# Optimization experiments

Measured on AMD Instinct MI355X. Metric: run time of the kernel, lower is better.

## Reference

```python
import jax, jax.numpy as jnp
import numpy as np

U = 256      # lstm_unit / embedding_fc_unit
V = 100000   # word vocab
WD = 300     # word embedding dim
PD = 64      # pos embedding dim
AD = 64      # action embedding dim
P = 50       # pos vocab
NA = 164     # 4 + 4*dep_num actions
B, T, K, L, S, A, DQ = 64, 128, 4, 128, 64, 64, 32
FORGET_BIAS = 1.0


def lstm_step(x, c, h, W, b):
    z = jnp.concatenate([x, h], -1) @ W + b
    i, j, f, o = jnp.split(z, 4, -1)
    nc = c * jax.nn.sigmoid(f + FORGET_BIAS) + jax.nn.sigmoid(i) * jnp.tanh(j)
    nh = jnp.tanh(nc) * jax.nn.sigmoid(o)
    return nc, nh


def run_lstm(xs, length, W, b):
    # xs: [B, L, D]; TF dynamic_rnn semantics: state frozen and output zeroed past length.
    Bn, Ln, _ = xs.shape
    u = W.shape[1] // 4
    def step(carry, tx):
        c, h = carry
        t, x = tx
        nc, nh = lstm_step(x, c, h, W, b)
        m = (t < length)[:, None]
        return (jnp.where(m, nc, c), jnp.where(m, nh, h)), jnp.where(m, nh, 0.0)
    init = (jnp.zeros((Bn, u), xs.dtype), jnp.zeros((Bn, u), xs.dtype))
    (cf, hf), outs = jax.lax.scan(step, init, (jnp.arange(Ln), jnp.swapaxes(xs, 0, 1)))
    return jnp.swapaxes(outs, 0, 1), (cf, hf)


def reverse_seq(xs, length):
    # tf.reverse_sequence: reverse first `length` steps, leave the rest in place.
    Ln = xs.shape[1]
    t = jnp.arange(Ln)[None, :]
    rev = jnp.where(t < length[:, None], length[:, None] - 1 - t, t)
    return jnp.take_along_axis(xs, rev[:, :, None], axis=1)


def forward(tree_word_id, tree_pos_id, token_word_id, token_pos_id, history_action_id,
            buff_top_id, deque_word_id, deque_pos_id, deque_length, children_order,
            stack_order, stack_length, token_length, history_action_length,
            word_emb, pos_emb, act_emb, wd_W, wd_b, tree_W, tree_b,
            stack0_W, stack0_b, stack1_W, stack1_b,
            fw0_W, fw0_b, bw0_W, bw0_b, fw1_W, fw1_b, bw1_W, bw1_b,
            act0_W, act0_b, act1_W, act1_b, dq0_W, dq0_b, dq1_W, dq1_b,
            fin_W, fin_b):
    Bn = tree_word_id.shape[0]

    def embed(wid, pid):
        e = jnp.concatenate([word_emb[wid], pos_emb[pid]], -1)
        return jax.nn.relu(e @ wd_W + wd_b)

    tree_e = embed(tree_word_id, tree_pos_id)       # [B, T, U]
    token_e = embed(token_word_id, token_pos_id)    # [B, L, U]
    deque_e = embed(deque_word_id, deque_pos_id)    # [B, DQ, U]
    hist_e = act_emb[history_action_id]             # [B, A, AD]

    # ---- tree LSTM over children structure ----
    Tn = tree_e.shape[1]
    Kn = children_order.shape[2]
    batch_col = jnp.arange(Bn)[:, None]
    H0 = jnp.zeros((Tn + 1, Bn, U), tree_e.dtype)
    C0 = jnp.zeros((Tn + 1, Bn, U), tree_e.dtype)

    def body(carry, i):
        H, C = carry
        idx = children_order[:, i]            # [B, K] indices into slots 0..i
        h = H[idx, batch_col]                 # [B, K, U]
        c = C[idx, batch_col]
        x = tree_e[:, i]                      # [B, U]
        hj = h.sum(1)
        ijo = jnp.concatenate([x, hj], -1) @ tree_W[:, :3 * U] + tree_b[:3 * U]
        xk = jnp.broadcast_to(x[:, None, :], (Bn, Kn, x.shape[-1]))
        f = jnp.concatenate([xk, h], -1) @ tree_W[:, 3 * U:] + tree_b[3 * U:]   # [B, K, U]
        ig, jg, og = jnp.split(ijo, 3, -1)
        nc = (c * jax.nn.sigmoid(f + FORGET_BIAS)).sum(1) + jax.nn.sigmoid(ig) * jnp.tanh(jg)
        nh = jnp.tanh(nc) * jax.nn.sigmoid(og)
        return (H.at[i + 1].set(nh), C.at[i + 1].set(nc)), None

    (H, _), _ = jax.lax.scan(body, (H0, C0), jnp.arange(Tn))
    stack_embedded = H[stack_order, batch_col]      # [B, S, U]

    # ---- stack LSTM (2-layer) ----
    o0, _ = run_lstm(stack_embedded, stack_length, stack0_W, stack0_b)
    _, (_, stack_h) = run_lstm(o0, stack_length, stack1_W, stack1_b)

    # ---- buff bi-LSTM (2 stacked bidirectional layers) ----
    fw0_o, _ = run_lstm(token_e, token_length, fw0_W, fw0_b)
    bw0_o, _ = run_lstm(reverse_seq(token_e, token_length), token_length, bw0_W, bw0_b)
    bw0_o = reverse_seq(bw0_o, token_length)
    x1 = jnp.concatenate([fw0_o, bw0_o], -1)
    fw1_o, (_, fw1_h) = run_lstm(x1, token_length, fw1_W, fw1_b)
    bw1_o, _ = run_lstm(reverse_seq(x1, token_length), token_length, bw1_W, bw1_b)
    bw1_o = reverse_seq(bw1_o, token_length)
    bidx = jnp.arange(Bn)
    fw_top = fw1_o[bidx, buff_top_id]
    bw_top = bw1_o[bidx, buff_top_id]
    bw_bottom = bw1_o[bidx, token_length - 1]
    buff_out = jnp.concatenate([fw1_h - fw_top, bw_top - bw_bottom], -1)

    # ---- action LSTM (2-layer) ----
    a0, _ = run_lstm(hist_e, history_action_length, act0_W, act0_b)
    _, (_, act_h) = run_lstm(a0, history_action_length, act1_W, act1_b)

    # ---- deque LSTM (2-layer) ----
    d0, _ = run_lstm(deque_e, deque_length, dq0_W, dq0_b)
    _, (_, dq_h) = run_lstm(d0, deque_length, dq1_W, dq1_b)

    feat = jnp.concatenate([stack_h, buff_out, act_h, dq_h], -1)   # [B, 5U]
    return jax.nn.relu(feat @ fin_W + fin_b)


def setup_inputs():
    key = jax.random.key(0)
    ks = jax.random.split(key, 48)
    r = lambda i, shape: jax.random.normal(ks[i], shape, jnp.float32) * 0.05
    ri = lambda i, shape, hi: jax.random.randint(ks[i], shape, 0, hi)
    inp = {}
    inp['tree_word_id'] = ri(0, (B, T), V)
    inp['tree_pos_id'] = ri(1, (B, T), P)
    inp['token_word_id'] = ri(2, (B, L), V)
    inp['token_pos_id'] = ri(3, (B, L), P)
    inp['history_action_id'] = ri(4, (B, A), NA)
    inp['buff_top_id'] = ri(5, (B,), L // 2)
    inp['deque_word_id'] = ri(6, (B, DQ), V)
    inp['deque_pos_id'] = ri(7, (B, DQ), P)
    inp['deque_length'] = jax.random.randint(ks[8], (B,), 1, DQ + 1)
    co = ri(9, (B, T, K), T)
    # a node may only reference already-computed children slots (<= step index)
    inp['children_order'] = jnp.minimum(co, jnp.arange(T)[None, :, None])
    inp['stack_order'] = ri(10, (B, S), T + 1)
    inp['stack_length'] = jax.random.randint(ks[11], (B,), 1, S + 1)
    inp['token_length'] = jax.random.randint(ks[12], (B,), L // 2, L + 1)
    inp['history_action_length'] = jax.random.randint(ks[13], (B,), 1, A + 1)
    inp['word_emb'] = r(14, (V, WD))
    inp['pos_emb'] = r(15, (P, PD))
    inp['act_emb'] = r(16, (NA, AD))
    inp['wd_W'] = r(17, (WD + PD, U)); inp['wd_b'] = jnp.zeros((U,))
    inp['tree_W'] = r(18, (2 * U, 4 * U)); inp['tree_b'] = jnp.zeros((4 * U,))
    inp['stack0_W'] = r(19, (2 * U, 4 * U)); inp['stack0_b'] = jnp.zeros((4 * U,))
    inp['stack1_W'] = r(20, (2 * U, 4 * U)); inp['stack1_b'] = jnp.zeros((4 * U,))
    inp['fw0_W'] = r(21, (2 * U, 4 * U)); inp['fw0_b'] = jnp.zeros((4 * U,))
    inp['bw0_W'] = r(22, (2 * U, 4 * U)); inp['bw0_b'] = jnp.zeros((4 * U,))
    inp['fw1_W'] = r(23, (3 * U, 4 * U)); inp['fw1_b'] = jnp.zeros((4 * U,))
    inp['bw1_W'] = r(24, (3 * U, 4 * U)); inp['bw1_b'] = jnp.zeros((4 * U,))
    inp['act0_W'] = r(25, (AD + U, 4 * U)); inp['act0_b'] = jnp.zeros((4 * U,))
    inp['act1_W'] = r(26, (2 * U, 4 * U)); inp['act1_b'] = jnp.zeros((4 * U,))
    inp['dq0_W'] = r(27, (2 * U, 4 * U)); inp['dq0_b'] = jnp.zeros((4 * U,))
    inp['dq1_W'] = r(28, (2 * U, 4 * U)); inp['dq1_b'] = jnp.zeros((4 * U,))
    inp['fin_W'] = r(29, (5 * U, NA)); inp['fin_b'] = jnp.zeros((NA,))
    return inp


def reference(tree_word_id, tree_pos_id, token_word_id, token_pos_id, history_action_id,
              buff_top_id, deque_word_id, deque_pos_id, deque_length, children_order,
              stack_order, stack_length, token_length, history_action_length,
              word_emb, pos_emb, act_emb, wd_W, wd_b, tree_W, tree_b,
              stack0_W, stack0_b, stack1_W, stack1_b,
              fw0_W, fw0_b, bw0_W, bw0_b, fw1_W, fw1_b, bw1_W, bw1_b,
              act0_W, act0_b, act1_W, act1_b, dq0_W, dq0_b, dq1_W, dq1_b,
              fin_W, fin_b):
    return forward(tree_word_id, tree_pos_id, token_word_id, token_pos_id, history_action_id,
                   buff_top_id, deque_word_id, deque_pos_id, deque_length, children_order,
                   stack_order, stack_length, token_length, history_action_length,
                   word_emb, pos_emb, act_emb, wd_W, wd_b, tree_W, tree_b,
                   stack0_W, stack0_b, stack1_W, stack1_b,
                   fw0_W, fw0_b, bw0_W, bw0_b, fw1_W, fw1_b, bw1_W, bw1_b,
                   act0_W, act0_b, act1_W, act1_b, dq0_W, dq0_b, dq1_W, dq1_b,
                   fin_W, fin_b)
```

## Files before the change

### kernel.cpp

```cpp
#include <hip/hip_runtime.h>
#include <hip/hip_bf16.h>
#include <hip/hip_fp16.h>
#include <cstdint>

#define BB   64
#define TT   128
#define KK   4
#define LL   128
#define SS   64
#define AA   64
#define DQN  32
#define UU   256
#define NAOUT 164
#define WDIM 300
#define PDIM 64
#define ADIM 64

#define OFF_TREE 0
#define OFF_S0   512
#define OFF_S1   1024
#define OFF_FW0  1536
#define OFF_BW0  2048
#define OFF_FW1  2560
#define OFF_BW1  3328
// ... 177 lines not shown
    __shared__ __align__(16) float s_e[384];
    if (p.flag[0] == 1) embed_impl<true>(p, s_e);
    else                embed_impl<false>(p, s_e);
}

template<int R>
__device__ __forceinline__ float lstm_step_f4(const float4* __restrict__ Wp,
                                              const float4 bz,
                                              const float* __restrict__ s_xh,
                                              float& c) {
    float zi = bz.x, zj = bz.y, zf = bz.z, zo = bz.w;
    for (int r0 = 0; r0 < R; r0 += 16) {
        float4 w[16];
        #pragma unroll
        for (int k = 0; k < 16; ++k) w[k] = Wp[(size_t)(r0 + k) * 256];
        __builtin_amdgcn_sched_barrier(0);
        #pragma unroll
        for (int q = 0; q < 4; ++q) {
            const float4 x4 = *reinterpret_cast<const float4*>(s_xh + r0 + 4 * q);
            const float xv[4] = {x4.x, x4.y, x4.z, x4.w};
            #pragma unroll
            for (int j = 0; j < 4; ++j) {
                const float4 wv = w[4 * q + j];
                zi = fmaf(xv[j], wv.x, zi);
                zj = fmaf(xv[j], wv.y, zj);
                zf = fmaf(xv[j], wv.z, zf);
                zo = fmaf(xv[j], wv.w, zo);
            }
        }
    }
    const float nc = c * sigm(zf) + sigm(zi) * tanhf(zj);
    c = nc;
    return tanhf(nc) * sigm(zo);
}

template<bool F32>
__device__ __forceinline__ float4 load_bias4(const void* b, int u) {
    return make_float4(ld1<F32>(b, u), ld1<F32>(b, 256 + u),
                       ld1<F32>(b, 512 + u) + 1.0f, ld1<F32>(b, 768 + u));
}

__device__ __forceinline__ float4 zx_load(const uint2* __restrict__ zx, size_t n, int u) {
    const uint2 v = zx[n * 256 + u];
    const float2 ij = unp2h(v.x);
    const float2 fo = unp2h(v.y);
    return make_float4(ij.x, ij.y, fo.x, fo.y);
}

template<bool F32>
__device__ void run_tree_f4(int b, const P& p, float* smem) {
    const int u = threadIdx.x;
    float* s_x  = smem;
    float* s_hj = smem + 256;
    float* s_hk = smem + 512;
    float* H = p.H;
    float* C = p.C;
    H[(size_t)b * UU + u] = 0.f;
    C[(size_t)b * UU + u] = 0.f;

    const float4* __restrict__ Wt = p.pkf + u;
    const float4* __restrict__ Wh = Wt + (size_t)256 * 256;
    const float bi = ld1<F32>(p.tree_b, u);
    const float bj = ld1<F32>(p.tree_b, 256 + u);
    const float bo = ld1<F32>(p.tree_b, 512 + u);
    const float bf = ld1<F32>(p.tree_b, 768 + u) + 1.0f;

// ... 48 lines not shown
                const float4 hj4 = *reinterpret_cast<const float4*>(s_hj + r);
                const float4 a0  = *reinterpret_cast<const float4*>(s_hk + r);
                const float4 a1  = *reinterpret_cast<const float4*>(s_hk + 256 + r);
                const float4 a2  = *reinterpret_cast<const float4*>(s_hk + 512 + r);
                const float4 a3  = *reinterpret_cast<const float4*>(s_hk + 768 + r);
                const float hjv[4] = {hj4.x, hj4.y, hj4.z, hj4.w};
                const float k0[4]  = {a0.x, a0.y, a0.z, a0.w};
                const float k1[4]  = {a1.x, a1.y, a1.z, a1.w};
                const float k2[4]  = {a2.x, a2.y, a2.z, a2.w};
                const float k3[4]  = {a3.x, a3.y, a3.z, a3.w};
                #pragma unroll
                for (int j = 0; j < 4; ++j) {
                    const float4 wv = w[4 * q + j];
                    zi = fmaf(hjv[j], wv.x, zi);
                    zj = fmaf(hjv[j], wv.y, zj);
                    zo = fmaf(hjv[j], wv.z, zo);
                    f0 = fmaf(k0[j], wv.w, f0);
                    f1 = fmaf(k1[j], wv.w, f1);
                    f2 = fmaf(k2[j], wv.w, f2);
                    f3 = fmaf(k3[j], wv.w, f3);
                }
            }
        }
        const float fsum = c0 * sigm(fx + f0) + c1 * sigm(fx + f1)
                         + c2 * sigm(fx + f2) + c3 * sigm(fx + f3);
        const float nc = fsum + sigm(zi) * tanhf(zj);
        const float nh = tanhf(nc) * sigm(zo);
        __syncthreads();
        H[((size_t)(i + 1) * BB + b) * UU + u] = nh;
        C[((size_t)(i + 1) * BB + b) * UU + u] = nc;
    }
}

template<bool F32>
__device__ void run_tree_hc(int b, const P& p, float* smem) {
    const int u = threadIdx.x;
    float* s_hj = smem;
    float* s_hk = smem + 256;
    float* H = p.H;
    float* C = p.C;
    H[(size_t)b * UU + u] = 0.f;
    C[(size_t)b * UU + u] = 0.f;
    const float4* __restrict__ Wh = p.pkf + (size_t)256 * 256 + u;

    for (int i = 0; i < TT; ++i) {
        const int* co = p.children_order + ((size_t)b * TT + i) * KK;
        const int i0 = co[0], i1 = co[1], i2 = co[2], i3 = co[3];
        const float h0 = H[((size_t)i0 * BB + b) * UU + u];
        const float h1 = H[((size_t)i1 * BB + b) * UU + u];
        const float h2 = H[((size_t)i2 * BB + b) * UU + u];
        const float h3 = H[((size_t)i3 * BB + b) * UU + u];
        const float c0 = C[((size_t)i0 * BB + b) * UU + u];
        const float c1 = C[((size_t)i1 * BB + b) * UU + u];
        const float c2 = C[((size_t)i2 * BB + b) * UU + u];
        const float c3 = C[((size_t)i3 * BB + b) * UU + u];
        s_hk[u]       = h0;
        s_hk[256 + u] = h1;
        s_hk[512 + u] = h2;
        s_hk[768 + u] = h3;
        s_hj[u]       = h0 + h1 + h2 + h3;
        __syncthreads();

        const float4 z0 = p.zxT[((size_t)b * TT + i) * 256 + u];
        float zi = z0.x, zj = z0.y, zo = z0.z, fx = z0.w;
        float f0 = 0.f, f1 = 0.f, f2 = 0.f, f3 = 0.f;
        for (int r0 = 0; r0 < 256; r0 += 16) {
            float4 w[16];
            #pragma unroll
            for (int k = 0; k < 16; ++k) w[k] = Wh[(size_t)(r0 + k) * 256];
            __builtin_amdgcn_sched_barrier(0);
            #pragma unroll
            for (int q = 0; q < 4; ++q) {
                const int r = r0 + 4 * q;
                const float4 hj4 = *reinterpret_cast<const float4*>(s_hj + r);
                const float4 a0  = *reinterpret_cast<const float4*>(s_hk + r);
                const float4 a1  = *reinterpret_cast<const float4*>(s_hk + 256 + r);
                const float4 a2  = *reinterpret_cast<const float4*>(s_hk + 512 + r);
                const float4 a3  = *reinterpret_cast<const float4*>(s_hk + 768 + r);
                const float hjv[4] = {hj4.x, hj4.y, hj4.z, hj4.w};
                const float k0[4]  = {a0.x, a0.y, a0.z, a0.w};
                const float k1[4]  = {a1.x, a1.y, a1.z, a1.w};
                const float k2[4]  = {a2.x, a2.y, a2.z, a2.w};
                const float k3[4]  = {a3.x, a3.y, a3.z, a3.w};
                #pragma unroll
                for (int j = 0; j < 4; ++j) {
                    const float4 wv = w[4 * q + j];
                    zi = fmaf(hjv[j], wv.x, zi);
                    zj = fmaf(hjv[j], wv.y, zj);
                    zo = fmaf(hjv[j], wv.z, zo);
                    f0 = fmaf(k0[j], wv.w, f0);
                    f1 = fmaf(k1[j], wv.w, f1);
                    f2 = fmaf(k2[j], wv.w, f2);
                    f3 = fmaf(k3[j], wv.w, f3);
                }
            }
        }
        const float fsum = c0 * sigm(fx + f0) + c1 * sigm(fx + f1)
                         + c2 * sigm(fx + f2) + c3 * sigm(fx + f3);
        const float nc = fsum + sigm(zi) * tanhf(zj);
        const float nh = tanhf(nc) * sigm(zo);
        __syncthreads();
        H[((size_t)(i + 1) * BB + b) * UU + u] = nh;
        C[((size_t)(i + 1) * BB + b) * UU + u] = nc;
    }
}

template<bool F32>
__device__ void run_token_l0_f4(int b, const P& p, float* smem, bool is_bw) {
    const int u = threadIdx.x;
    float* s_xh = smem;
    const int len = p.token_length[b];
    const float4* __restrict__ Wp = p.pkf + (size_t)(is_bw ? OFF_BW0 : OFF_FW0) * 256 + u;
    const float4 bz = load_bias4<F32>(is_bw ? p.bw0_b : p.fw0_b, u);

    float c0 = 0.f;
    s_xh[256 + u] = 0.f;
    for (int t = 0; t < len; ++t) {
        const int row = is_bw ? (len - 1 - t) : t;
        s_xh[u] = bf2f(p.token_e[((size_t)b * LL + row) * UU + u]);
        __syncthreads();
        const float nh = lstm_step_f4<512>(Wp, bz, s_xh, c0);
        p.x1[((size_t)b * LL + row) * 512 + (is_bw ? 256 : 0) + u] = f2bf(nh);
        __syncthreads();
        s_xh[256 + u] = nh;
    }
}

template<bool F32>
__device__ void run_act_dq_f4(int b, const P& p, float* smem) {
    const int u = threadIdx.x;
    float* s_xh0 = smem;
    float* s_xh1 = smem + 512;

    {
        const int len = p.history_action_length[b];
        const float4* __restrict__ W0 = p.pkf + (size_t)OFF_ACT0 * 256 + u;
// ... 429 lines not shown
    float c = 0.f, hlast = 0.f;
    s_h[u] = 0.f;
    __syncthreads();
    for (int t = 0; t < len; ++t) {
        const float4 bz = zx_load(p.zxC, (size_t)b * AA + t, u);
        const float nh = lstm_step_f4<256>(Wh, bz, s_h, c);
        __syncthreads();
        s_h[u] = nh;
        __syncthreads();
        hlast = nh;
    }
    p.act_h[b * UU + u] = hlast;
}

template<bool F32>
__device__ void chain_dq1(int b, const P& p, float* s_h) {
    const int u = threadIdx.x;
    const int len = p.deque_length[b];
    const float4* __restrict__ Wh = p.pkf + (size_t)PKH_DQ1 * 256 + u;
    float c = 0.f, hlast = 0.f;
    s_h[u] = 0.f;
    __syncthreads();
    for (int t = 0; t < len; ++t) {
        const float4 bz = zx_load(p.zxD, (size_t)b * DQN + t, u);
        const float nh = lstm_step_f4<256>(Wh, bz, s_h, c);
        __syncthreads();
        s_h[u] = nh;
        __syncthreads();
        hlast = nh;
    }
    p.dq_h[b * UU + u] = hlast;
}

template<bool F32>
__device__ void p1b_impl(const P& p, float* smem) {
    const int chain = blockIdx.x >> 6;
    const int b     = blockIdx.x & 63;
    if (chain == 0)      run_tree_f4<F32>(b, p, smem);
    else if (chain == 1) chain_token_l0<F32>(b, p, smem, false);
    else if (chain == 2) chain_token_l0<F32>(b, p, smem, true);
    else if (chain == 3) chain_act0<F32>(b, p, smem);
    else                 chain_dq0<F32>(b, p, smem);
}

__global__ __launch_bounds__(256) void p1b_kernel(P p) {
    __shared__ __align__(16) float smem[1536];
    if (p.flag[0] == 1) p1b_impl<true>(p, smem);
    else                p1b_impl<false>(p, smem);
}

template<bool F32>
__device__ void p2b_impl(const P& p, float* smem) {
    const int chain = blockIdx.x >> 6;
    const int b     = blockIdx.x & 63;
    if (chain == 0)      chain_fw1<F32>(b, p, smem);
    else if (chain == 1) chain_bw1<F32>(b, p, smem);
    else if (chain == 2) chain_stack0<F32>(b, p, smem);
    else if (chain == 3) chain_act1<F32>(b, p, smem);
    else                 chain_dq1<F32>(b, p, smem);
}

__global__ __launch_bounds__(256) void p2b_kernel(P p) {
    __shared__ __align__(16) float smem[256];
    if (p.flag[0] == 1) p2b_impl<true>(p, smem);
    else                p2b_impl<false>(p, smem);
}

template<bool F32>
__device__ void p1c_impl(const P& p, float* smem) {
    const int s = blockIdx.x & 7;
    const int j = blockIdx.x >> 3;
    if (s == 0 || s == 5) {
        if (j >= 32) return;
        run_tree_hc<F32>((s == 5 ? 32 : 0) + j, p, smem);
    } else if (s == 1 || s == 6) {
        if (j >= 32) return;
        chain_token_l0<F32>((s == 6 ? 32 : 0) + j, p, smem, false);
    } else if (s == 2 || s == 7) {
        if (j >= 32) return;
        chain_token_l0<F32>((s == 7 ? 32 : 0) + j, p, smem, true);
    } else if (s == 3) {
        chain_act0<F32>(j, p, smem);
    } else {
        chain_dq0<F32>(j, p, smem);
    }
}

__global__ __launch_bounds__(256) void p1c_kernel(P p) {
    __shared__ __align__(16) float smem[1280];
    if (p.flag[0] == 1) p1c_impl<true>(p, smem);
    else                p1c_impl<false>(p, smem);
}

template<bool F32>
__device__ void p2c_impl(const P& p, float* smem) {
    const int s = blockIdx.x & 7;
    const int j = blockIdx.x >> 3;
    if (s == 0 || s == 5) {
        if (j >= 32) return;
        chain_fw1<F32>((s == 5 ? 32 : 0) + j, p, smem);
    } else if (s == 1 || s == 6) {
        if (j >= 32) return;
        chain_bw1<F32>((s == 6 ? 32 : 0) + j, p, smem);
    } else if (s == 2 || s == 7) {
        if (j >= 32) return;
        chain_stack0<F32>((s == 7 ? 32 : 0) + j, p, smem);
    } else if (s == 3) {
        chain_act1<F32>(j, p, smem);
    } else {
        chain_dq1<F32>(j, p, smem);
    }
}

__global__ __launch_bounds__(256) void p2c_kernel(P p) {
    __shared__ __align__(16) float smem[256];
    if (p.flag[0] == 1) p2c_impl<true>(p, smem);
    else                p2c_impl<false>(p, smem);
}

template<bool F32>
__device__ void p3_impl(const P& p, float* smem) {
    const int b = blockIdx.x;
    const int u = threadIdx.x;
    const int len = p.stack_length[b];
    const float4* __restrict__ Wh = p.pkf + (size_t)PKH_S1 * 256 + u;
    float c = 0.f, hlast = 0.f;
    smem[u] = 0.f;
    __syncthreads();
    for (int t = 0; t < len; ++t) {
        const float4 bz = zx_load(p.zxS, (size_t)b * SS + t, u);
        const float nh = lstm_step_f4<256>(Wh, bz, smem, c);
        __syncthreads();
        smem[u] = nh;
        __syncthreads();
        hlast = nh;
    }
    p.stack_h[b * UU + u] = hlast;
}

__global__ __launch_bounds__(256) void p3_kernel(P p) {
    __shared__ __align__(16) float smem[256];
    if (p.flag[0] == 1) p3_impl<true>(p, smem);
    else                p3_impl<false>(p, smem);
}

template<bool F32>
__device__ __forceinline__ void st_out(void* out, int i, float v) {
    if constexpr (F32) reinterpret_cast<float*>(out)[i] = v;
    else               reinterpret_cast<__hip_bfloat16*>(out)[i] = __float2bfloat16(v);
}

template<bool F32>
__device__ void final_impl(const P& p, void* out, float* s_f) {
    const int b = blockIdx.x;
    const int u = threadIdx.x;
    s_f[u]        = p.stack_h[b * UU + u];
    s_f[256 + u]  = p.fw1_h[b * UU + u] - p.fw_top[b * UU + u];
    s_f[512 + u]  = p.bw_top[b * UU + u] - p.bw_bottom[b * UU + u];
    s_f[768 + u]  = p.act_h[b * UU + u];
    s_f[1024 + u] = p.dq_h[b * UU + u];
    __syncthreads();
    if (u < NAOUT) {
        float acc = ld1<F32>(p.fin_b, u);
        for (int r = 0; r < 1280; ++r)
            acc = fmaf(s_f[r], ld1<F32>(p.fin_W, (size_t)r * NAOUT + u), acc);
        acc = fmaxf(acc, 0.f);
        st_out<F32>(out, b * NAOUT + u, acc);
    }
    if (b == 0 && u == 0) {
        const uint_t POIS = 0xAAAAAAAAu;
        const uint_t* te = reinterpret_cast<const uint_t*>(p.tree_e);
        const uint_t* x1 = reinterpret_cast<const uint_t*>(p.x1);
        const uint_t* sh = reinterpret_cast<const uint_t*>(p.stack_h);
        bool te_p = true, x1_p = true;
        for (int i = 0; i < 8; ++i) { te_p &= (te[i] == POIS); x1_p &= (x1[i] == POIS); }
        bool sh_p = (sh[0] == POIS) && (sh[1] == POIS);
// ... 67 lines not shown
    p.dq1_W    = d_in[39];
    p.dq1_b    = d_in[40];
    p.fin_W    = d_in[41];
    p.fin_b    = d_in[42];

    char* base = (char*)d_ws;

    size_t off = 0;
    p.flag = (int*)(base + off);           off += 256;
    p.stack_h   = (float*)(base + off);    off += (size_t)BB * UU * 4;
    p.fw1_h     = (float*)(base + off);    off += (size_t)BB * UU * 4;
    p.fw_top    = (float*)(base + off);    off += (size_t)BB * UU * 4;
    p.bw_top    = (float*)(base + off);    off += (size_t)BB * UU * 4;
    p.bw_bottom = (float*)(base + off);    off += (size_t)BB * UU * 4;
    p.act_h     = (float*)(base + off);    off += (size_t)BB * UU * 4;
    p.dq_h      = (float*)(base + off);    off += (size_t)BB * UU * 4;
    p.tree_e  = (float*)(base + off);      off += (size_t)BB * TT * UU * 4;
    p.token_e = (ushort_t*)(base + off);   off += (size_t)BB * LL * UU * 2;
    p.deque_e = (ushort_t*)(base + off);   off += (size_t)BB * DQN * UU * 2;
    p.x1      = (ushort_t*)(base + off);   off += (size_t)BB * LL * 512 * 2;
    p.a0_seq  = (float*)(base + off);      off += (size_t)BB * AA * UU * 4;
    p.d0_seq  = (float*)(base + off);      off += (size_t)BB * DQN * UU * 4;
    p.s0_seq  = (float*)(base + off);      off += (size_t)BB * SS * UU * 4;
    p.H       = (float*)(base + off);      off += (size_t)(TT + 1) * BB * UU * 4;
    p.C       = (float*)(base + off);      off += (size_t)(TT + 1) * BB * UU * 4;
    p.zxA     = (uint2*)(base + off);      off += (size_t)BB * LL * UU * 8;
    p.zxB     = (uint2*)(base + off);      off += (size_t)BB * LL * UU * 8;
    p.zxC     = (uint2*)(base + off);      off += (size_t)BB * AA * UU * 8;
    p.zxD     = (uint2*)(base + off);      off += (size_t)BB * DQN * UU * 8;
    p.zxS     = (uint2*)(base + off);      off += (size_t)BB * SS * UU * 8;
    p.pkf     = (float4*)(base + off);     off += (size_t)PK_ROWS_B * 256 * 16;
    const size_t planB_size = off;
    p.zxT     = (float4*)(base + off);     off += (size_t)BB * TT * UU * 16;
    const size_t planC_size = off;

    if (ws_size >= planC_size) {
        detect_kernel<<<1, 64, 0, stream>>>((const uint_t*)d_in[14], p.flag);
        pack_h_kernel<<<dim3(PK_ROWS_B), dim3(256), 0, stream>>>(p);
        embed_kernel<<<dim3(BB * TT + BB * LL + BB * DQN), dim3(256), 0, stream>>>(p);
        xpre0_kernel<<<dim3(960), dim3(256), 0, stream>>>(p);
        p1c_kernel<<<dim3(512), dim3(256), 0, stream>>>(p);
        xpre1_kernel<<<dim3(832), dim3(256), 0, stream>>>(p);
        p2c_kernel<<<dim3(512), dim3(256), 0, stream>>>(p);
        xpre2_kernel<<<dim3(128), dim3(256), 0, stream>>>(p);
        p3_kernel<<<dim3(BB), dim3(256), 0, stream>>>(p);
        final_kernel<<<dim3(BB), dim3(256), 0, stream>>>(p, d_out);
        return;
    }

    if (ws_size >= planB_size) {
        p.zxT = (float4*)base;
        detect_kernel<<<1, 64, 0, stream>>>((const uint_t*)d_in[14], p.flag);
        pack_h_kernel<<<dim3(PK_ROWS_B), dim3(256), 0, stream>>>(p);
        embed_kernel<<<dim3(BB * TT + BB * LL + BB * DQN), dim3(256), 0, stream>>>(p);
        xpre0_kernel<<<dim3(704), dim3(256), 0, stream>>>(p);
        p1b_kernel<<<dim3(5 * BB), dim3(256), 0, stream>>>(p);
        xpre1_kernel<<<dim3(832), dim3(256), 0, stream>>>(p);
        p2b_kernel<<<dim3(5 * BB), dim3(256), 0, stream>>>(p);
        xpre2_kernel<<<dim3(128), dim3(256), 0, stream>>>(p);
        p3_kernel<<<dim3(BB), dim3(256), 0, stream>>>(p);
        final_kernel<<<dim3(BB), dim3(256), 0, stream>>>(p, d_out);
        return;
    }

    off = 0;
    p.flag = (int*)(base + off);           off += 16;
    p.stack_h   = (float*)(base + off);    off += (size_t)BB * UU * 4;
    p.fw1_h     = (float*)(base + off);    off += (size_t)BB * UU * 4;
    p.fw_top    = (float*)(base + off);    off += (size_t)BB * UU * 4;
    p.bw_top    = (float*)(base + off);    off += (size_t)BB * UU * 4;
    p.bw_bottom = (float*)(base + off);    off += (size_t)BB * UU * 4;
    p.act_h     = (float*)(base + off);    off += (size_t)BB * UU * 4;
    p.dq_h      = (float*)(base + off);    off += (size_t)BB * UU * 4;
    p.tree_e  = (float*)(base + off);      off += (size_t)BB * TT * UU * 4;
    p.token_e = (ushort_t*)(base + off);   off += (size_t)BB * LL * UU * 2;
    p.deque_e = (ushort_t*)(base + off);   off += (size_t)BB * DQN * UU * 2;
    p.x1      = (ushort_t*)(base + off);   off += (size_t)BB * LL * 512 * 2;
    p.H       = (float*)(base + off);      off += (size_t)(TT + 1) * BB * UU * 4;
    p.C       = (float*)(base + off);      off += (size_t)(TT + 1) * BB * UU * 4;
    p.pkf     = (float4*)(base + off);     off += (size_t)PK_ROWS_FB * 256 * 16;
    p.a0_seq = p.d0_seq = p.s0_seq = (float*)base;
    p.zxA = p.zxB = p.zxC = p.zxD = p.zxS = (uint2*)base;
    p.zxT = (float4*)base;

    if (ws_size < off) {
        sentinel_kernel<<<1, 64, 0, stream>>>(d_out, 7000.f + (float)(ws_size >> 20));
        return;
    }

    detect_kernel<<<1, 64, 0, stream>>>((const uint_t*)d_in[14], p.flag);
    pack_fb_kernel<<<dim3(PK_ROWS_FB), dim3(256), 0, stream>>>(p);
    embed_kernel<<<dim3(BB * TT + BB * LL + BB * DQN), dim3(256), 0, stream>>>(p);
    phase1_fb_kernel<<<dim3(4 * BB), dim3(256), 0, stream>>>(p);
// ... 4 lines not shown
```

Measured before the change: 5.103 ms.

## Batch multiple sequences per block in recurrent LSTM chains to reuse weights

Each recurrent chain kernel now processes several batch elements per block (2 for the tree LSTM, 4 for the sequence LSTMs), so every recurrent-weight load is reused across G hidden states instead of one. The intent is to cut the weight bandwidth from global or L2 per step, which dominates these latency-bound recurrences. In exchange, grouped sequences run to the maximum length in the group, register pressure rises, and fewer blocks are launched, which lowers parallelism across CUs.

```diff
diff --git a/kernel.cpp b/kernel.cpp
--- a/kernel.cpp
+++ b/kernel.cpp
@@ -233,6 +233,37 @@
     const float nc = c * sigm(zf) + sigm(zi) * tanhf(zj);
     c = nc;
     return tanhf(nc) * sigm(zo);
+}
+
+template<int G>
+__device__ __forceinline__ void lstm_accum_g(const float4* __restrict__ Wp,
+                                             const float4* bzg,
+                                             const float* __restrict__ s_h,
+                                             float4* acc) {
+    #pragma unroll
+    for (int g = 0; g < G; ++g) acc[g] = bzg[g];
+    for (int r0 = 0; r0 < 256; r0 += 8) {
+        float4 w[8];
+        #pragma unroll
+        for (int k = 0; k < 8; ++k) w[k] = Wp[(size_t)(r0 + k) * 256];
+        __builtin_amdgcn_sched_barrier(0);
+        #pragma unroll
+        for (int g = 0; g < G; ++g) {
+            #pragma unroll
+            for (int q = 0; q < 2; ++q) {
+                const float4 x4 = *reinterpret_cast<const float4*>(s_h + g * 256 + r0 + 4 * q);
+                const float xv[4] = {x4.x, x4.y, x4.z, x4.w};
+                #pragma unroll
+                for (int j = 0; j < 4; ++j) {
+                    const float4 wv = w[4 * q + j];
+                    acc[g].x = fmaf(xv[j], wv.x, acc[g].x);
+                    acc[g].y = fmaf(xv[j], wv.y, acc[g].y);
+                    acc[g].z = fmaf(xv[j], wv.z, acc[g].z);
+                    acc[g].w = fmaf(xv[j], wv.w, acc[g].w);
+                }
+            }
+        }
+    }
 }
 
 template<bool F32>
@@ -347,76 +378,94 @@
     }
 }
 
-template<bool F32>
-__device__ void run_tree_hc(int b, const P& p, float* smem) {
+template<bool F32, int G>
+__device__ void run_tree_hg(int b0, const P& p, float* smem) {
     const int u = threadIdx.x;
     float* s_hj = smem;
-    float* s_hk = smem + 256;
+    float* s_hk = smem + G * 256;
     float* H = p.H;
     float* C = p.C;
-    H[(size_t)b * UU + u] = 0.f;
-    C[(size_t)b * UU + u] = 0.f;
+    #pragma unroll
+    for (int g = 0; g < G; ++g) {
+        H[(size_t)(b0 + g) * UU + u] = 0.f;
+        C[(size_t)(b0 + g) * UU + u] = 0.f;
+    }
     const float4* __restrict__ Wh = p.pkf + (size_t)256 * 256 + u;
 
     for (int i = 0; i < TT; ++i) {
-        const int* co = p.children_order + ((size_t)b * TT + i) * KK;
-        const int i0 = co[0], i1 = co[1], i2 = co[2], i3 = co[3];
-        const float h0 = H[((size_t)i0 * BB + b) * UU + u];
-        const float h1 = H[((size_t)i1 * BB + b) * UU + u];
-        const float h2 = H[((size_t)i2 * BB + b) * UU + u];
-        const float h3 = H[((size_t)i3 * BB + b) * UU + u];
-        const float c0 = C[((size_t)i0 * BB + b) * UU + u];
-        const float c1 = C[((size_t)i1 * BB + b) * UU + u];
-        const float c2 = C[((size_t)i2 * BB + b) * UU + u];
-        const float c3 = C[((size_t)i3 * BB + b) * UU + u];
-        s_hk[u]       = h0;
-        s_hk[256 + u] = h1;
-        s_hk[512 + u] = h2;
-        s_hk[768 + u] = h3;
-        s_hj[u]       = h0 + h1 + h2 + h3;
-        __syncthreads();
-
-        const float4 z0 = p.zxT[((size_t)b * TT + i) * 256 + u];
-        float zi = z0.x, zj = z0.y, zo = z0.z, fx = z0.w;
-        float f0 = 0.f, f1 = 0.f, f2 = 0.f, f3 = 0.f;
-        for (int r0 = 0; r0 < 256; r0 += 16) {
-            float4 w[16];
+        float c0[G], c1[G], c2[G], c3[G];
+        #pragma unroll
+        for (int g = 0; g < G; ++g) {
+            const int b = b0 + g;
+            const int* co = p.children_order + ((size_t)b * TT + i) * KK;
+            const int i0 = co[0], i1 = co[1], i2 = co[2], i3 = co[3];
+            const float h0 = H[((size_t)i0 * BB + b) * UU + u];
+            const float h1 = H[((size_t)i1 * BB + b) * UU + u];
+            const float h2 = H[((size_t)i2 * BB + b) * UU + u];
+            const float h3 = H[((size_t)i3 * BB + b) * UU + u];
+            c0[g] = C[((size_t)i0 * BB + b) * UU + u];
+            c1[g] = C[((size_t)i1 * BB + b) * UU + u];
+            c2[g] = C[((size_t)i2 * BB + b) * UU + u];
+            c3[g] = C[((size_t)i3 * BB + b) * UU + u];
+            s_hk[g * 1024 + u]       = h0;
+            s_hk[g * 1024 + 256 + u] = h1;
+            s_hk[g * 1024 + 512 + u] = h2;
+            s_hk[g * 1024 + 768 + u] = h3;
+            s_hj[g * 256 + u]        = h0 + h1 + h2 + h3;
+        }
+        __syncthreads();
+
+        float zi[G], zj[G], zo[G], fx[G], f0[G], f1[G], f2[G], f3[G];
+        #pragma unroll
+        for (int g = 0; g < G; ++g) {
+            const float4 z0 = p.zxT[((size_t)(b0 + g) * TT + i) * 256 + u];
+            zi[g] = z0.x; zj[g] = z0.y; zo[g] = z0.z; fx[g] = z0.w;
+            f0[g] = 0.f; f1[g] = 0.f; f2[g] = 0.f; f3[g] = 0.f;
+        }
+        for (int r0 = 0; r0 < 256; r0 += 8) {
+            float4 w[8];
             #pragma unroll
-            for (int k = 0; k < 16; ++k) w[k] = Wh[(size_t)(r0 + k) * 256];
+            for (int k = 0; k < 8; ++k) w[k] = Wh[(size_t)(r0 + k) * 256];
             __builtin_amdgcn_sched_barrier(0);
             #pragma unroll
-            for (int q = 0; q < 4; ++q) {
-                const int r = r0 + 4 * q;
-                const float4 hj4 = *reinterpret_cast<const float4*>(s_hj + r);
-                const float4 a0  = *reinterpret_cast<const float4*>(s_hk + r);
-                const float4 a1  = *reinterpret_cast<const float4*>(s_hk + 256 + r);
-                const float4 a2  = *reinterpret_cast<const float4*>(s_hk + 512 + r);
-                const float4 a3  = *reinterpret_cast<const float4*>(s_hk + 768 + r);
-                const float hjv[4] = {hj4.x, hj4.y, hj4.z, hj4.w};
-                const float k0[4]  = {a0.x, a0.y, a0.z, a0.w};
-                const float k1[4]  = {a1.x, a1.y, a1.z, a1.w};
-                const float k2[4]  = {a2.x, a2.y, a2.z, a2.w};
-                const float k3[4]  = {a3.x, a3.y, a3.z, a3.w};
+            for (int g = 0; g < G; ++g) {
                 #pragma unroll
-                for (int j = 0; j < 4; ++j) {
-                    const float4 wv = w[4 * q + j];
-                    zi = fmaf(hjv[j], wv.x, zi);
-                    zj = fmaf(hjv[j], wv.y, zj);
-                    zo = fmaf(hjv[j], wv.z, zo);
-                    f0 = fmaf(k0[j], wv.w, f0);
-                    f1 = fmaf(k1[j], wv.w, f1);
-                    f2 = fmaf(k2[j], wv.w, f2);
-                    f3 = fmaf(k3[j], wv.w, f3);
+                for (int q = 0; q < 2; ++q) {
+                    const int r = r0 + 4 * q;
+                    const float4 hj4 = *reinterpret_cast<const float4*>(s_hj + g * 256 + r);
+                    const float4 a0  = *reinterpret_cast<const float4*>(s_hk + g * 1024 + r);
+                    const float4 a1  = *reinterpret_cast<const float4*>(s_hk + g * 1024 + 256 + r);
+                    const float4 a2  = *reinterpret_cast<const float4*>(s_hk + g * 1024 + 512 + r);
+                    const float4 a3  = *reinterpret_cast<const float4*>(s_hk + g * 1024 + 768 + r);
+                    const float hjv[4] = {hj4.x, hj4.y, hj4.z, hj4.w};
+                    const float k0[4]  = {a0.x, a0.y, a0.z, a0.w};
+                    const float k1[4]  = {a1.x, a1.y, a1.z, a1.w};
+                    const float k2[4]  = {a2.x, a2.y, a2.z, a2.w};
+                    const float k3[4]  = {a3.x, a3.y, a3.z, a3.w};
+                    #pragma unroll
+                    for (int j = 0; j < 4; ++j) {
+                        const float4 wv = w[4 * q + j];
+                        zi[g] = fmaf(hjv[j], wv.x, zi[g]);
+                        zj[g] = fmaf(hjv[j], wv.y, zj[g]);
+                        zo[g] = fmaf(hjv[j], wv.z, zo[g]);
+                        f0[g] = fmaf(k0[j], wv.w, f0[g]);
+                        f1[g] = fmaf(k1[j], wv.w, f1[g]);
+                        f2[g] = fmaf(k2[j], wv.w, f2[g]);
+                        f3[g] = fmaf(k3[j], wv.w, f3[g]);
+                    }
                 }
             }
         }
-        const float fsum = c0 * sigm(fx + f0) + c1 * sigm(fx + f1)
-                         + c2 * sigm(fx + f2) + c3 * sigm(fx + f3);
-        const float nc = fsum + sigm(zi) * tanhf(zj);
-        const float nh = tanhf(nc) * sigm(zo);
-        __syncthreads();
-        H[((size_t)(i + 1) * BB + b) * UU + u] = nh;
-        C[((size_t)(i + 1) * BB + b) * UU + u] = nc;
+        __syncthreads();
+        #pragma unroll
+        for (int g = 0; g < G; ++g) {
+            const float fsum = c0[g] * sigm(fx[g] + f0[g]) + c1[g] * sigm(fx[g] + f1[g])
+                             + c2[g] * sigm(fx[g] + f2[g]) + c3[g] * sigm(fx[g] + f3[g]);
+            const float nc = fsum + sigm(zi[g]) * tanhf(zj[g]);
+            const float nh = tanhf(nc) * sigm(zo[g]);
+            H[((size_t)(i + 1) * BB + (b0 + g)) * UU + u] = nh;
+            C[((size_t)(i + 1) * BB + (b0 + g)) * UU + u] = nc;
+        }
     }
 }
 
@@ -912,6 +961,341 @@
     p.dq_h[b * UU + u] = hlast;
 }
 
+template<int G>
+__device__ __forceinline__ void gates_g(const float4* acc, const bool* valid,
+                                        float* c, float* nh) {
+    #pragma unroll
+    for (int g = 0; g < G; ++g) {
+        if (valid[g]) {
+            const float nc = c[g] * sigm(acc[g].z) + sigm(acc[g].x) * tanhf(acc[g].y);
+            c[g] = nc;
+            nh[g] = tanhf(nc) * sigm(acc[g].w);
+        }
+    }
+}
+
+template<bool F32, int G>
+__device__ void chain_token_l0_g(int b0, const P& p, float* s_h, bool bw) {
+    const int u = threadIdx.x;
+    const float4* __restrict__ Wh = p.pkf + (size_t)(bw ? PKH_BW0 : PKH_FW0) * 256 + u;
+    const uint2* zx = bw ? p.zxB : p.zxA;
+    int len[G]; float c[G]; int maxlen = 1;
+    #pragma unroll
+    for (int g = 0; g < G; ++g) {
+        len[g] = p.token_length[b0 + g];
+        c[g] = 0.f;
+        s_h[g * 256 + u] = 0.f;
+        if (len[g] > maxlen) maxlen = len[g];
+    }
+    __syncthreads();
+    for (int t = 0; t < maxlen; ++t) {
+        float4 bzg[G]; bool valid[G]; int row[G];
+        #pragma unroll
+        for (int g = 0; g < G; ++g) {
+            valid[g] = (t < len[g]);
+            row[g] = valid[g] ? (bw ? len[g] - 1 - t : t) : 0;
+            bzg[g] = zx_load(zx, (size_t)(b0 + g) * LL + row[g], u);
+        }
+        float4 acc[G];
+        lstm_accum_g<G>(Wh, bzg, s_h, acc);
+        float nh[G];
+        gates_g<G>(acc, valid, c, nh);
+        #pragma unroll
+        for (int g = 0; g < G; ++g)
+            if (valid[g])
+                p.x1[((size_t)(b0 + g) * LL + row[g]) * 512 + (bw ? 256 : 0) + u] = f2bf(nh[g]);
+        __syncthreads();
+        #pragma unroll
+        for (int g = 0; g < G; ++g) if (valid[g]) s_h[g * 256 + u] = nh[g];
+        __syncthreads();
+    }
+}
+
+template<bool F32, int G>
+__device__ void chain_act0_g(int b0, const P& p, float* s_h) {
+    const int u = threadIdx.x;
+    const float4* __restrict__ Wh = p.pkf + (size_t)PKH_ACT0 * 256 + u;
+    int len[G]; float c[G]; int maxlen = 1;
+    #pragma unroll
+    for (int g = 0; g < G; ++g) {
+        len[g] = p.history_action_length[b0 + g];
+        c[g] = 0.f;
+        s_h[g * 256 + u] = 0.f;
+        if (len[g] > maxlen) maxlen = len[g];
+    }
+    __syncthreads();
+    for (int t = 0; t < maxlen; ++t) {
+        float4 bzg[G]; bool valid[G];
+        #pragma unroll
+        for (int g = 0; g < G; ++g) {
+            valid[g] = (t < len[g]);
+            const int tt = valid[g] ? t : 0;
+            bzg[g] = zx_load(p.zxC, (size_t)(b0 + g) * AA + tt, u);
+        }
+        float4 acc[G];
+        lstm_accum_g<G>(Wh, bzg, s_h, acc);
+        float nh[G];
+        gates_g<G>(acc, valid, c, nh);
+        #pragma unroll
+        for (int g = 0; g < G; ++g)
+            if (valid[g]) p.a0_seq[((size_t)(b0 + g) * AA + t) * UU + u] = nh[g];
+        __syncthreads();
+        #pragma unroll
+        for (int g = 0; g < G; ++g) if (valid[g]) s_h[g * 256 + u] = nh[g];
+        __syncthreads();
+    }
+}
+
+template<bool F32, int G>
+__device__ void chain_dq0_g(int b0, const P& p, float* s_h) {
+    const int u = threadIdx.x;
+    const float4* __restrict__ Wh = p.pkf + (size_t)PKH_DQ0 * 256 + u;
+    int len[G]; float c[G]; int maxlen = 1;
+    #pragma unroll
+    for (int g = 0; g < G; ++g) {
+        len[g] = p.deque_length[b0 + g];
+        c[g] = 0.f;
+        s_h[g * 256 + u] = 0.f;
+        if (len[g] > maxlen) maxlen = len[g];
+    }
+    __syncthreads();
+    for (int t = 0; t < maxlen; ++t) {
+        float4 bzg[G]; bool valid[G];
+        #pragma unroll
+        for (int g = 0; g < G; ++g) {
+            valid[g] = (t < len[g]);
+            const int tt = valid[g] ? t : 0;
+            bzg[g] = zx_load(p.zxD, (size_t)(b0 + g) * DQN + tt, u);
+        }
+        float4 acc[G];
+        lstm_accum_g<G>(Wh, bzg, s_h, acc);
+        float nh[G];
+        gates_g<G>(acc, valid, c, nh);
+        #pragma unroll
+        for (int g = 0; g < G; ++g)
+            if (valid[g]) p.d0_seq[((size_t)(b0 + g) * DQN + t) * UU + u] = nh[g];
+        __syncthreads();
+        #pragma unroll
+        for (int g = 0; g < G; ++g) if (valid[g]) s_h[g * 256 + u] = nh[g];
+        __syncthreads();
+    }
+}
+
+template<bool F32, int G>
+__device__ void chain_fw1_g(int b0, const P& p, float* s_h) {
+    const int u = threadIdx.x;
+    const float4* __restrict__ Wh = p.pkf + (size_t)PKH_FW1 * 256 + u;
+    int len[G], btop[G]; float c[G]; int maxlen = 1;
+    #pragma unroll
+    for (int g = 0; g < G; ++g) {
+        len[g]  = p.token_length[b0 + g];
+        btop[g] = p.buff_top_id[b0 + g];
+        c[g] = 0.f;
+        s_h[g * 256 + u] = 0.f;
+        if (len[g] > maxlen) maxlen = len[g];
+    }
+    __syncthreads();
+    for (int t = 0; t < maxlen; ++t) {
+        float4 bzg[G]; bool valid[G];
+        #pragma unroll
+        for (int g = 0; g < G; ++g) {
+            valid[g] = (t < len[g]);
+            const int tt = valid[g] ? t : 0;
+            bzg[g] = zx_load(p.zxA, (size_t)(b0 + g) * LL + tt, u);
+        }
+        float4 acc[G];
+        lstm_accum_g<G>(Wh, bzg, s_h, acc);
+        float nh[G];
+        gates_g<G>(acc, valid, c, nh);
+        #pragma unroll
+        for (int g = 0; g < G; ++g)
+            if (valid[g] && t == btop[g]) p.fw_top[(b0 + g) * UU + u] = nh[g];
+        __syncthreads();
+        #pragma unroll
+        for (int g = 0; g < G; ++g) if (valid[g]) s_h[g * 256 + u] = nh[g];
+        __syncthreads();
+    }
+    #pragma unroll
+    for (int g = 0; g < G; ++g) p.fw1_h[(b0 + g) * UU + u] = s_h[g * 256 + u];
+}
+
+template<bool F32, int G>
+__device__ void chain_bw1_g(int b0, const P& p, float* s_h) {
+    const int u = threadIdx.x;
+    const float4* __restrict__ Wh = p.pkf + (size_t)PKH_BW1 * 256 + u;
+    int len[G], btop[G]; float c[G]; int maxlen = 1;
+    #pragma unroll
+    for (int g = 0; g < G; ++g) {
+        len[g]  = p.token_length[b0 + g];
+        btop[g] = p.buff_top_id[b0 + g];
+        c[g] = 0.f;
+        s_h[g * 256 + u] = 0.f;
+        if (len[g] > maxlen) maxlen = len[g];
+    }
+    __syncthreads();
+    for (int t = 0; t < maxlen; ++t) {
+        float4 bzg[G]; bool valid[G];
+        #pragma unroll
+        for (int g = 0; g < G; ++g) {
+            valid[g] = (t < len[g]);
+            const int row = valid[g] ? (len[g] - 1 - t) : 0;
+            bzg[g] = zx_load(p.zxB, (size_t)(b0 + g) * LL + row, u);
+        }
+        float4 acc[G];
+        lstm_accum_g<G>(Wh, bzg, s_h, acc);
+        float nh[G];
+        gates_g<G>(acc, valid, c, nh);
+        #pragma unroll
+        for (int g = 0; g < G; ++g) {
+            if (valid[g]) {
+                if (t == 0)                      p.bw_bottom[(b0 + g) * UU + u] = nh[g];
+                if (t == len[g] - 1 - btop[g])   p.bw_top[(b0 + g) * UU + u]    = nh[g];
+            }
+        }
+        __syncthreads();
+        #pragma unroll
+        for (int g = 0; g < G; ++g) if (valid[g]) s_h[g * 256 + u] = nh[g];
+        __syncthreads();
+    }
+}
+
+template<bool F32, int G>
+__device__ void chain_stack0_g(int b0, const P& p, float* s_h) {
+    const int u = threadIdx.x;
+    const float4* __restrict__ Wh = p.pkf + (size_t)PKH_S0 * 256 + u;
+    int len[G]; float c[G]; int maxlen = 1;
+    #pragma unroll
+    for (int g = 0; g < G; ++g) {
+        len[g] = p.stack_length[b0 + g];
+        c[g] = 0.f;
+        s_h[g * 256 + u] = 0.f;
+        if (len[g] > maxlen) maxlen = len[g];
+    }
+    __syncthreads();
+    for (int t = 0; t < maxlen; ++t) {
+        float4 bzg[G]; bool valid[G];
+        #pragma unroll
+        for (int g = 0; g < G; ++g) {
+            valid[g] = (t < len[g]);
+            const int tt = valid[g] ? t : 0;
+            bzg[g] = zx_load(p.zxS, (size_t)(b0 + g) * SS + tt, u);
+        }
+        float4 acc[G];
+        lstm_accum_g<G>(Wh, bzg, s_h, acc);
+        float nh[G];
+        gates_g<G>(acc, valid, c, nh);
+        #pragma unroll
+        for (int g = 0; g < G; ++g)
+            if (valid[g]) p.s0_seq[((size_t)(b0 + g) * SS + t) * UU + u] = nh[g];
+        __syncthreads();
+        #pragma unroll
+        for (int g = 0; g < G; ++g) if (valid[g]) s_h[g * 256 + u] = nh[g];
+        __syncthreads();
+    }
+}
+
+template<bool F32, int G>
+__device__ void chain_act1_g(int b0, const P& p, float* s_h) {
+    const int u = threadIdx.x;
+    const float4* __restrict__ Wh = p.pkf + (size_t)PKH_ACT1 * 256 + u;
+    int len[G]; float c[G]; int maxlen = 1;
+    #pragma unroll
+    for (int g = 0; g < G; ++g) {
+        len[g] = p.history_action_length[b0 + g];
+        c[g] = 0.f;
+        s_h[g * 256 + u] = 0.f;
+        if (len[g] > maxlen) maxlen = len[g];
+    }
+    __syncthreads();
+    for (int t = 0; t < maxlen; ++t) {
+        float4 bzg[G]; bool valid[G];
+        #pragma unroll
+        for (int g = 0; g < G; ++g) {
+            valid[g] = (t < len[g]);
+            const int tt = valid[g] ? t : 0;
+            bzg[g] = zx_load(p.zxC, (size_t)(b0 + g) * AA + tt, u);
+        }
+        float4 acc[G];
+        lstm_accum_g<G>(Wh, bzg, s_h, acc);
+        float nh[G];
+        gates_g<G>(acc, valid, c, nh);
+        __syncthreads();
+        #pragma unroll
+        for (int g = 0; g < G; ++g) if (valid[g]) s_h[g * 256 + u] = nh[g];
+        __syncthreads();
+    }
+    #pragma unroll
+    for (int g = 0; g < G; ++g) p.act_h[(b0 + g) * UU + u] = s_h[g * 256 + u];
+}
+
+template<bool F32, int G>
+__device__ void chain_dq1_g(int b0, const P& p, float* s_h) {
+    const int u = threadIdx.x;
+    const float4* __restrict__ Wh = p.pkf + (size_t)PKH_DQ1 * 256 + u;
+    int len[G]; float c[G]; int maxlen = 1;
+    #pragma unroll
+    for (int g = 0; g < G; ++g) {
+        len[g] = p.deque_length[b0 + g];
+        c[g] = 0.f;
+        s_h[g * 256 + u] = 0.f;
+        if (len[g] > maxlen) maxlen = len[g];
+    }
+    __syncthreads();
+    for (int t = 0; t < maxlen; ++t) {
+        float4 bzg[G]; bool valid[G];
+        #pragma unroll
+        for (int g = 0; g < G; ++g) {
+            valid[g] = (t < len[g]);
+            const int tt = valid[g] ? t : 0;
+            bzg[g] = zx_load(p.zxD, (size_t)(b0 + g) * DQN + tt, u);
+        }
+        float4 acc[G];
+        lstm_accum_g<G>(Wh, bzg, s_h, acc);
+        float nh[G];
+        gates_g<G>(acc, valid, c, nh);
+        __syncthreads();
+        #pragma unroll
+        for (int g = 0; g < G; ++g) if (valid[g]) s_h[g * 256 + u] = nh[g];
+        __syncthreads();
+    }
+    #pragma unroll
+    for (int g = 0; g < G; ++g) p.dq_h[(b0 + g) * UU + u] = s_h[g * 256 + u];
+}
+
+template<bool F32, int G>
+__device__ void chain_stack1_g(int b0, const P& p, float* s_h) {
+    const int u = threadIdx.x;
+    const float4* __restrict__ Wh = p.pkf + (size_t)PKH_S1 * 256 + u;
+    int len[G]; float c[G]; int maxlen = 1;
+    #pragma unroll
+    for (int g = 0; g < G; ++g) {
+        len[g] = p.stack_length[b0 + g];
+        c[g] = 0.f;
+        s_h[g * 256 + u] = 0.f;
+        if (len[g] > maxlen) maxlen = len[g];
+    }
+    __syncthreads();
+    for (int t = 0; t < maxlen; ++t) {
+        float4 bzg[G]; bool valid[G];
+        #pragma unroll
+        for (int g = 0; g < G; ++g) {
+            valid[g] = (t < len[g]);
+            const int tt = valid[g] ? t : 0;
+            bzg[g] = zx_load(p.zxS, (size_t)(b0 + g) * SS + tt, u);
+        }
+        float4 acc[G];
+        lstm_accum_g<G>(Wh, bzg, s_h, acc);
+        float nh[G];
+        gates_g<G>(acc, valid, c, nh);
+        __syncthreads();
+        #pragma unroll
+        for (int g = 0; g < G; ++g) if (valid[g]) s_h[g * 256 + u] = nh[g];
+        __syncthreads();
+    }
+    #pragma unroll
+    for (int g = 0; g < G; ++g) p.stack_h[(b0 + g) * UU + u] = s_h[g * 256 + u];
+}
+
 template<bool F32>
 __device__ void p1b_impl(const P& p, float* smem) {
     const int chain = blockIdx.x >> 6;
@@ -947,59 +1331,7 @@
 }
 
 template<bool F32>
-__device__ void p1c_impl(const P& p, float* smem) {
-    const int s = blockIdx.x & 7;
-    const int j = blockIdx.x >> 3;
-    if (s == 0 || s == 5) {
-        if (j >= 32) return;
-        run_tree_hc<F32>((s == 5 ? 32 : 0) + j, p, smem);
-    } else if (s == 1 || s == 6) {
-        if (j >= 32) return;
-        chain_token_l0<F32>((s == 6 ? 32 : 0) + j, p, smem, false);
-    } else if (s == 2 || s == 7) {
-        if (j >= 32) return;
-        chain_token_l0<F32>((s == 7 ? 32 : 0) + j, p, smem, true);
-    } else if (s == 3) {
-        chain_act0<F32>(j, p, smem);
-    } else {
-        chain_dq0<F32>(j, p, smem);
-    }
-}
-
-__global__ __launch_bounds__(256) void p1c_kernel(P p) {
-    __shared__ __align__(16) float smem[1280];
-    if (p.flag[0] == 1) p1c_impl<true>(p, smem);
-    else                p1c_impl<false>(p, smem);
-}
-
-template<bool F32>
-__device__ void p2c_impl(const P& p, float* smem) {
-    const int s = blockIdx.x & 7;
-    const int j = blockIdx.x >> 3;
-    if (s == 0 || s == 5) {
-        if (j >= 32) return;
-        chain_fw1<F32>((s == 5 ? 32 : 0) + j, p, smem);
-    } else if (s == 1 || s == 6) {
-        if (j >= 32) return;
-        chain_bw1<F32>((s == 6 ? 32 : 0) + j, p, smem);
-    } else if (s == 2 || s == 7) {
-        if (j >= 32) return;
-        chain_stack0<F32>((s == 7 ? 32 : 0) + j, p, smem);
-    } else if (s == 3) {
-        chain_act1<F32>(j, p, smem);
-    } else {
-        chain_dq1<F32>(j, p, smem);
-    }
-}
-
-__global__ __launch_bounds__(256) void p2c_kernel(P p) {
-    __shared__ __align__(16) float smem[256];
-    if (p.flag[0] == 1) p2c_impl<true>(p, smem);
-    else                p2c_impl<false>(p, smem);
-}
-
-template<bool F32>
-__device__ void p3_impl(const P& p, float* smem) {
+__device__ void p3b_impl(const P& p, float* smem) {
     const int b = blockIdx.x;
     const int u = threadIdx.x;
     const int len = p.stack_length[b];
@@ -1018,10 +1350,75 @@
     p.stack_h[b * UU + u] = hlast;
 }
 
-__global__ __launch_bounds__(256) void p3_kernel(P p) {
+__global__ __launch_bounds__(256) void p3b_kernel(P p) {
     __shared__ __align__(16) float smem[256];
-    if (p.flag[0] == 1) p3_impl<true>(p, smem);
-    else                p3_impl<false>(p, smem);
+    if (p.flag[0] == 1) p3b_impl<true>(p, smem);
+    else                p3b_impl<false>(p, smem);
+}
+
+template<bool F32>
+__device__ void p1d_impl(const P& p, float* smem) {
+    const int s = blockIdx.x & 7;
+    const int j = blockIdx.x >> 3;
+    if (s == 0 || s == 4) {
+        if (j >= 16) return;
+        run_tree_hg<F32, 2>((s == 4 ? 32 : 0) + 2 * j, p, smem);
+    } else if (s == 1 || s == 5) {
+        if (j >= 8) return;
+        chain_token_l0_g<F32, 4>((s == 5 ? 32 : 0) + 4 * j, p, smem, false);
+    } else if (s == 2 || s == 6) {
+        if (j >= 8) return;
+        chain_token_l0_g<F32, 4>((s == 6 ? 32 : 0) + 4 * j, p, smem, true);
+    } else if (s == 3) {
+        if (j >= 16) return;
+        chain_act0_g<F32, 4>(4 * j, p, smem);
+    } else {
+        if (j >= 16) return;
+        chain_dq0_g<F32, 4>(4 * j, p, smem);
+    }
+}
+
+__global__ __launch_bounds__(256) void p1d_kernel(P p) {
+    __shared__ __align__(16) float smem[2560];
+    if (p.flag[0] == 1) p1d_impl<true>(p, smem);
+    else                p1d_impl<false>(p, smem);
+}
+
+template<bool F32>
+__device__ void p2d_impl(const P& p, float* smem) {
+    const int s = blockIdx.x & 7;
+    const int j = blockIdx.x >> 3;
+    if (s == 0 || s == 4) {
+        if (j >= 8) return;
+        chain_fw1_g<F32, 4>((s == 4 ? 32 : 0) + 4 * j, p, smem);
+    } else if (s == 1 || s == 5) {
+        if (j >= 8) return;
+        chain_bw1_g<F32, 4>((s == 5 ? 32 : 0) + 4 * j, p, smem);
+    } else if (s == 2 || s == 6) {
+        if (j >= 8) return;
+        chain_stack0_g<F32, 4>((s == 6 ? 32 : 0) + 4 * j, p, smem);
+    } else if (s == 3) {
+        chain_act1_g<F32, 4>(4 * j, p, smem);
+    } else {
+        chain_dq1_g<F32, 4>(4 * j, p, smem);
+    }
+}
+
+__global__ __launch_bounds__(256) void p2d_kernel(P p) {
+    __shared__ __align__(16) float smem[1024];
+    if (p.flag[0] == 1) p2d_impl<true>(p, smem);
+    else                p2d_impl<false>(p, smem);
+}
+
+template<bool F32>
+__device__ void p3d_impl(const P& p, float* smem) {
+    chain_stack1_g<F32, 4>(4 * blockIdx.x, p, smem);
+}
+
+__global__ __launch_bounds__(256) void p3d_kernel(P p) {
+    __shared__ __align__(16) float smem[1024];
+    if (p.flag[0] == 1) p3d_impl<true>(p, smem);
+    else                p3d_impl<false>(p, smem);
 }
 
 template<bool F32>
@@ -1155,18 +1552,18 @@
     p.pkf     = (float4*)(base + off);     off += (size_t)PK_ROWS_B * 256 * 16;
     const size_t planB_size = off;
     p.zxT     = (float4*)(base + off);     off += (size_t)BB * TT * UU * 16;
-    const size_t planC_size = off;
-
-    if (ws_size >= planC_size) {
+    const size_t planD_size = off;
+
+    if (ws_size >= planD_size) {
         detect_kernel<<<1, 64, 0, stream>>>((const uint_t*)d_in[14], p.flag);
         pack_h_kernel<<<dim3(PK_ROWS_B), dim3(256), 0, stream>>>(p);
         embed_kernel<<<dim3(BB * TT + BB * LL + BB * DQN), dim3(256), 0, stream>>>(p);
         xpre0_kernel<<<dim3(960), dim3(256), 0, stream>>>(p);
-        p1c_kernel<<<dim3(512), dim3(256), 0, stream>>>(p);
+        p1d_kernel<<<dim3(256), dim3(256), 0, stream>>>(p);
         xpre1_kernel<<<dim3(832), dim3(256), 0, stream>>>(p);
-        p2c_kernel<<<dim3(512), dim3(256), 0, stream>>>(p);
+        p2d_kernel<<<dim3(128), dim3(256), 0, stream>>>(p);
         xpre2_kernel<<<dim3(128), dim3(256), 0, stream>>>(p);
-        p3_kernel<<<dim3(BB), dim3(256), 0, stream>>>(p);
+        p3d_kernel<<<dim3(16), dim3(256), 0, stream>>>(p);
         final_kernel<<<dim3(BB), dim3(256), 0, stream>>>(p, d_out);
         return;
     }
@@ -1181,7 +1578,7 @@
         xpre1_kernel<<<dim3(832), dim3(256), 0, stream>>>(p);
         p2b_kernel<<<dim3(5 * BB), dim3(256), 0, stream>>>(p);
         xpre2_kernel<<<dim3(128), dim3(256), 0, stream>>>(p);
-        p3_kernel<<<dim3(BB), dim3(256), 0, stream>>>(p);
+        p3b_kernel<<<dim3(BB), dim3(256), 0, stream>>>(p);
         final_kernel<<<dim3(BB), dim3(256), 0, stream>>>(p, d_out);
         return;
     }
```

Result: slower. 6.246 ms (+22.4%).
